# Optimization experiments

Hardware: AMD Instinct MI355X
Metric: run time of the kernel (lower is better)

Reference implementation:

```python
import jax, jax.numpy as jnp
import numpy as np

NS_C = 128
VDW_N = 6.0
MAX_VDW = 0.0356
MIN_VDW = 0.0178
DEV_VDW_RADIUS = 0.2
DM_MIN = 0.5


def _mlp(h, W1, b1, W2, b2):
    # h: [B, Nl, Nt, 2*ns_c] -> [B, Nl, Nt]
    r = jax.nn.relu(jnp.einsum('blnc,ck->blnk', h, W1) + b1)
    return (jnp.einsum('blnk,k->bln', r, W2[:, 0]) + b2[0])


def setup_inputs() -> dict:
    key = jax.random.key(0)
    ks = jax.random.split(key, 16)
    B, Nl, Nt, C = 8, 64, 512, NS_C
    s1 = 1.0 / np.sqrt(2 * C)
    s2 = 1.0 / np.sqrt(C)
    return {
        'ligand_pos': jax.random.normal(ks[0], (B, Nl, 3), jnp.float32),
        'target_pos': jax.random.normal(ks[1], (B, Nt, 3), jnp.float32),
        'ligand_vdw_radii': jax.random.uniform(ks[2], (B, Nl), jnp.float32),
        'target_vdw_radii': jax.random.uniform(ks[3], (B, Nt), jnp.float32),
        'ligand_non_metal': jnp.ones((B, Nl), jnp.float32),
        'target_non_metal': jnp.ones((B, Nt), jnp.float32),
        'interaction_indice': jax.random.uniform(ks[4], (B, 3, Nl, Nt), jnp.float32),
        'rotor': jax.random.uniform(ks[5], (B,), jnp.float32),
        'h_cat': jax.random.normal(ks[6], (B, Nl, Nt, 2 * C), jnp.float32),
        'WA1': jax.random.normal(ks[7], (2 * C, C), jnp.float32) * s1,
        'bA1': jnp.zeros((C,), jnp.float32),
        'WA2': jax.random.normal(ks[8], (C, 1), jnp.float32) * s2,
        'bA2': jnp.zeros((1,), jnp.float32),
        'WB1': jax.random.normal(ks[9], (2 * C, C), jnp.float32) * s1,
        'bB1': jnp.zeros((C,), jnp.float32),
        'WB2': jax.random.normal(ks[10], (C, 1), jnp.float32) * s2,
        'bB2': jnp.zeros((1,), jnp.float32),
        'hbond_coeff': jnp.array([1.0], jnp.float32),
        'hydrophobic_coeff': jnp.array([0.5], jnp.float32),
        'rotor_coeff': jnp.array([0.5], jnp.float32),
    }


def reference(ligand_pos, target_pos, ligand_vdw_radii, target_vdw_radii,
              ligand_non_metal, target_non_metal, interaction_indice, rotor,
              h_cat, WA1, bA1, WA2, bA2, WB1, bB1, WB2, bB2,
              hbond_coeff, hydrophobic_coeff, rotor_coeff):
    # pairwise distance matrix [B, Nl, Nt]
    diff = ligand_pos[:, :, None, :] - target_pos[:, None, :, :]
    dm = jnp.sqrt(jnp.sum(diff * diff, axis=-1) + 1e-10)
    dm = jnp.where(dm < DM_MIN, jnp.float32(1e10), dm)

    # shared pair quantities (computed once, fused)
    Bp = jnp.tanh(_mlp(h_cat, WB1, bB1, WB2, bB2)) * DEV_VDW_RADIUS
    dm_0 = ligand_vdw_radii[:, :, None] + target_vdw_radii[:, None, :] + Bp

    # vdw term
    dm_0c = jnp.where(dm_0 < 1e-4, jnp.float32(1.0), dm_0)
    r6 = (dm_0c / dm) ** VDW_N
    vdw_e = jnp.minimum(r6 * r6 - 2.0 * r6, 100.0)
    vdw_e = vdw_e * ligand_non_metal[:, :, None] * target_non_metal[:, None, :]
    A_vdw = jax.nn.sigmoid(_mlp(h_cat, WA1, bA1, WA2, bA2))
    A_vdw = A_vdw * (MAX_VDW - MIN_VDW) + MIN_VDW
    vdw = jnp.sum(A_vdw * vdw_e, axis=(1, 2))

    d = dm - dm_0

    def hbond_term(A, coeff):
        r = jnp.clip(d * A / -0.7, 0.0, 1.0)
        return jnp.sum(r, axis=(1, 2)) * -(coeff[0] * coeff[0])

    hbond = hbond_term(interaction_indice[:, 0], hbond_coeff)
    metal = hbond_term(interaction_indice[:, 1], hbond_coeff)

    hphob = jnp.clip((-d + 1.5) * interaction_indice[:, 2], 0.0, 1.0)
    hphob = jnp.sum(hphob, axis=(1, 2)) * -(hydrophobic_coeff[0] * hydrophobic_coeff[0])

    energies = jnp.stack([vdw, hbond, metal, hphob], axis=-1)  # [B, 4]
    energies = energies / (1.0 + rotor_coeff[0] * rotor_coeff[0] * rotor[:, None])
    return energies
```

## Files before the change

kernel.cpp:

```cpp
#include <hip/hip_runtime.h>
#include <hip/hip_bf16.h>


typedef _Float16 half8 __attribute__((ext_vector_type(8)));
typedef float    f32x4 __attribute__((ext_vector_type(4)));
typedef unsigned int u32x4 __attribute__((ext_vector_type(4)));

#define NLIG 64
#define NTGT 512
#define KDIM 256
#define NDIM 256
#define BM   128
#define BK   32
#define NKS  8
#define RS   40

__global__ void ed_prep_kernel(const float* __restrict__ WA1,
                               const float* __restrict__ WB1,
                               _Float16* __restrict__ wt,
                               float* __restrict__ out) {
    int gid = blockIdx.x * 256 + threadIdx.x;
    int c   = gid >> 6;
    int n0  = (gid & 63) * 4;
    const float* src = (n0 < 128) ? (WA1 + c * 128 + n0)
                                  : (WB1 + c * 128 + (n0 - 128));
    f32x4 v = *(const f32x4*)src;
#pragma unroll
    for (int j = 0; j < 4; ++j)
        wt[(size_t)(n0 + j) * 256 + c] = (_Float16)v[j];
    if (gid < 32) out[gid] = 0.0f;
}

__global__ __launch_bounds__(512, 4) void ed_main_kernel(
    const float* __restrict__ lig_pos, const float* __restrict__ tgt_pos,
    const float* __restrict__ lig_vdw, const float* __restrict__ tgt_vdw,
    const float* __restrict__ lig_nm,  const float* __restrict__ tgt_nm,
    const float* __restrict__ ind,     const float* __restrict__ rotor,
    const float* __restrict__ h,       const _Float16* __restrict__ wt,
    const float* __restrict__ bA1, const float* __restrict__ WA2,
    const float* __restrict__ bA2,
    const float* __restrict__ bB1, const float* __restrict__ WB2,
    const float* __restrict__ bB2,
    const float* __restrict__ hbc, const float* __restrict__ hpc,
    const float* __restrict__ rtc,
    float* __restrict__ out)
{
    __shared__ _Float16 sA[2][BM * RS];
    __shared__ _Float16 sW[2][NDIM * RS];
    __shared__ float    sRed[4][BM];
    __shared__ float    sFin[32];

    const int tid  = threadIdx.x;
    const int lane = tid & 63;
    const int wid  = tid >> 6;
    const int wm   = wid >> 2;
    const int wn   = wid & 3;
    const int lr   = lane & 15;
    const int lg   = lane >> 4;

    const int bx = blockIdx.x;
    const int b  = bx >> 8;
    const int l  = (bx >> 2) & 63;
    const int t0 = (bx & 3) * BM;

    const float* hA = h + (size_t)bx * (BM * KDIM);

    const int arow = tid >> 2;
    const int akq  = (tid & 3) * 8;
    const int wrow = tid >> 1;
    const int whq  = (tid & 1) * 16;

    f32x4 a0, a1;
    u32x4 w0, w1;

    {
        const float* pa = hA + (size_t)arow * KDIM + akq;
        a0 = *(const f32x4*)pa;
        a1 = *(const f32x4*)(pa + 4);
        const _Float16* pw = wt + wrow * KDIM + whq;
        w0 = *(const u32x4*)pw;
        w1 = *(const u32x4*)(pw + 8);
        half8 hv;
#pragma unroll
        for (int j = 0; j < 4; ++j) hv[j] = (_Float16)a0[j];
#pragma unroll
        for (int j = 0; j < 4; ++j) hv[4 + j] = (_Float16)a1[j];
        *(half8*)&sA[0][arow * RS + akq] = hv;
        *(u32x4*)&sW[0][wrow * RS + whq]     = w0;
        *(u32x4*)&sW[0][wrow * RS + whq + 8] = w1;
    }

    f32x4 acc[4][4];
#pragma unroll
    for (int m = 0; m < 4; ++m)
#pragma unroll
        for (int n = 0; n < 4; ++n) acc[m][n] = 0;

    for (int ks = 0; ks < NKS; ++ks) {
        const int bf = ks & 1;
        __syncthreads();
        if (ks + 1 < NKS) {
            const float* pa = hA + (size_t)arow * KDIM + (ks + 1) * BK + akq;
            a0 = *(const f32x4*)pa;
            a1 = *(const f32x4*)(pa + 4);
            const _Float16* pw = wt + wrow * KDIM + (ks + 1) * BK + whq;
            w0 = *(const u32x4*)pw;
            w1 = *(const u32x4*)(pw + 8);
        }
        half8 af[4], wf[4];
#pragma unroll
        for (int m = 0; m < 4; ++m)
            af[m] = *(const half8*)&sA[bf][(wm * 64 + m * 16 + lr) * RS + lg * 8];
#pragma unroll
        for (int n = 0; n < 4; ++n)
            wf[n] = *(const half8*)&sW[bf][(wn * 64 + n * 16 + lr) * RS + lg * 8];
#pragma unroll
        for (int m = 0; m < 4; ++m)
#pragma unroll
            for (int n = 0; n < 4; ++n)
                acc[m][n] = __builtin_amdgcn_mfma_f32_16x16x32_f16(
                    af[m], wf[n], acc[m][n], 0, 0, 0);
        if (ks + 1 < NKS) {
            const int nb = bf ^ 1;
            half8 hv;
#pragma unroll
            for (int j = 0; j < 4; ++j) hv[j] = (_Float16)a0[j];
#pragma unroll
            for (int j = 0; j < 4; ++j) hv[4 + j] = (_Float16)a1[j];
            *(half8*)&sA[nb][arow * RS + akq] = hv;
            *(u32x4*)&sW[nb][wrow * RS + whq]     = w0;
            *(u32x4*)&sW[nb][wrow * RS + whq + 8] = w1;
        }
    }

    float cb[4], cw[4];
#pragma unroll
    for (int n = 0; n < 4; ++n) {
        int col = wn * 64 + n * 16 + lr;
        if (col < 128) { cb[n] = bA1[col];       cw[n] = WA2[col]; }
        else           { cb[n] = bB1[col - 128]; cw[n] = WB2[col - 128]; }
    }
#pragma unroll
    for (int m = 0; m < 4; ++m) {
#pragma unroll
        for (int r = 0; r < 4; ++r) {
            float p = 0.f;
#pragma unroll
            for (int n = 0; n < 4; ++n)
                p += fmaxf(acc[m][n][r] + cb[n], 0.f) * cw[n];
            p += __shfl_xor(p, 1);
            p += __shfl_xor(p, 2);
            p += __shfl_xor(p, 4);
            p += __shfl_xor(p, 8);
            if (lr == 0)
                sRed[wn][wm * 64 + m * 16 + lg * 4 + r] = p;
        }
    }
    __syncthreads();

    float e0 = 0.f, e1 = 0.f, e2 = 0.f, e3 = 0.f;
    if (tid < BM) {
        const int t = t0 + tid;
        float mlpA = sRed[0][tid] + sRed[1][tid] + bA2[0];
        float mlpB = sRed[2][tid] + sRed[3][tid] + bB2[0];
        float Bp = tanhf(mlpB) * 0.2f;
        float lv = lig_vdw[b * NLIG + l];
        float tv = tgt_vdw[b * NTGT + t];
        float dx = lig_pos[(b * NLIG + l) * 3 + 0] - tgt_pos[(b * NTGT + t) * 3 + 0];
        float dy = lig_pos[(b * NLIG + l) * 3 + 1] - tgt_pos[(b * NTGT + t) * 3 + 1];
        float dz = lig_pos[(b * NLIG + l) * 3 + 2] - tgt_pos[(b * NTGT + t) * 3 + 2];
        float dm = sqrtf(dx * dx + dy * dy + dz * dz + 1e-10f);
        if (dm < 0.5f) dm = 1e10f;
        float dm0  = lv + tv + Bp;
        float dm0c = (dm0 < 1e-4f) ? 1.0f : dm0;
        float qr = dm0c / dm;
        float q2 = qr * qr;
        float r6 = q2 * q2 * q2;
        float ve = fminf(r6 * r6 - 2.0f * r6, 100.0f);
        ve *= lig_nm[b * NLIG + l] * tgt_nm[b * NTGT + t];
        float Av = 1.0f / (1.0f + expf(-mlpA)) * (float)(0.0356 - 0.0178) + 0.0178f;
        e0 = Av * ve;
        float d = dm - dm0;
        const float* ib = ind + (size_t)b * 3 * NLIG * NTGT + (size_t)l * NTGT + t;
        float i0 = ib[0];
        float i1 = ib[NLIG * NTGT];
        float i2 = ib[2 * NLIG * NTGT];
        e1 = fminf(fmaxf(d * i0 / -0.7f, 0.f), 1.f);
        e2 = fminf(fmaxf(d * i1 / -0.7f, 0.f), 1.f);
        e3 = fminf(fmaxf((-d + 1.5f) * i2, 0.f), 1.f);
    }
#pragma unroll
    for (int off = 32; off > 0; off >>= 1) {
        e0 += __shfl_down(e0, off);
        e1 += __shfl_down(e1, off);
        e2 += __shfl_down(e2, off);
        e3 += __shfl_down(e3, off);
    }
    if (lane == 0) {
        sFin[wid * 4 + 0] = e0; sFin[wid * 4 + 1] = e1;
        sFin[wid * 4 + 2] = e2; sFin[wid * 4 + 3] = e3;
    }
    __syncthreads();
    if (tid == 0) {
        float s0 = 0, s1 = 0, s2 = 0, s3 = 0;
#pragma unroll
        for (int w = 0; w < 8; ++w) {
            s0 += sFin[w * 4 + 0]; s1 += sFin[w * 4 + 1];
            s2 += sFin[w * 4 + 2]; s3 += sFin[w * 4 + 3];
        }
        float hc = hbc[0], pc = hpc[0], rc = rtc[0];
        float inv = 1.0f / (1.0f + rc * rc * rotor[b]);
        __hip_atomic_fetch_add(&out[b * 4 + 0], s0 * inv,
                               __ATOMIC_RELAXED, __HIP_MEMORY_SCOPE_AGENT);
        __hip_atomic_fetch_add(&out[b * 4 + 1], -(hc * hc) * s1 * inv,
                               __ATOMIC_RELAXED, __HIP_MEMORY_SCOPE_AGENT);
        __hip_atomic_fetch_add(&out[b * 4 + 2], -(hc * hc) * s2 * inv,
                               __ATOMIC_RELAXED, __HIP_MEMORY_SCOPE_AGENT);
        __hip_atomic_fetch_add(&out[b * 4 + 3], -(pc * pc) * s3 * inv,
                               __ATOMIC_RELAXED, __HIP_MEMORY_SCOPE_AGENT);
    }
}

extern "C" void kernel_launch(void* const* d_in, const int* in_sizes, int n_in,
                              void* d_out, int out_size, void* d_ws, size_t ws_size,
                              hipStream_t stream) {
    (void)in_sizes; (void)n_in; (void)out_size; (void)ws_size;
    const float* lig_pos = (const float*)d_in[0];
    const float* tgt_pos = (const float*)d_in[1];
    const float* lig_vdw = (const float*)d_in[2];
    const float* tgt_vdw = (const float*)d_in[3];
    const float* lig_nm  = (const float*)d_in[4];
    const float* tgt_nm  = (const float*)d_in[5];
    const float* ind     = (const float*)d_in[6];
    const float* rotor   = (const float*)d_in[7];
    const float* h       = (const float*)d_in[8];
    const float* WA1     = (const float*)d_in[9];
    const float* bA1     = (const float*)d_in[10];
    const float* WA2     = (const float*)d_in[11];
    const float* bA2     = (const float*)d_in[12];
    const float* WB1     = (const float*)d_in[13];
    const float* bB1     = (const float*)d_in[14];
    const float* WB2     = (const float*)d_in[15];
    const float* bB2     = (const float*)d_in[16];
    const float* hbc     = (const float*)d_in[17];
    const float* hpc     = (const float*)d_in[18];
    const float* rtc     = (const float*)d_in[19];
    float* out  = (float*)d_out;
    _Float16* wt = (_Float16*)d_ws;

    ed_prep_kernel<<<dim3(64), dim3(256), 0, stream>>>(WA1, WB1, wt, out);
    ed_main_kernel<<<dim3(2048), dim3(512), 0, stream>>>(
        lig_pos, tgt_pos, lig_vdw, tgt_vdw, lig_nm, tgt_nm, ind, rotor, h, wt,
        bA1, WA2, bA2, bB1, WB2, bB2, hbc, hpc, rtc, out);
}
```

Baseline: 463.6 us.

## Drop LDS staging and stream h directly into MFMA registers with 3-deep prefetch

The GEMM no longer stages the h tile and the weights through double-buffered shared memory. Each wave now loads its A fragments straight from global memory into registers, using a three-stage register prefetch, and reads the fp16 weight fragments directly from global memory or cache. Blocks shrink to 256 threads covering 64 target rows, so there are twice as many blocks, and each wave computes a 32x128 tile that covers one full MLP. The aim is to remove LDS traffic and block-wide barriers in a kernel that is bound by memory bandwidth. The cost is redundant weight reads from global memory and higher register pressure.

```diff
diff --git a/kernel.cpp b/kernel.cpp
--- a/kernel.cpp
+++ b/kernel.cpp
@@ -4,16 +4,10 @@
 
 typedef _Float16 half8 __attribute__((ext_vector_type(8)));
 typedef float    f32x4 __attribute__((ext_vector_type(4)));
-typedef unsigned int u32x4 __attribute__((ext_vector_type(4)));
 
 #define NLIG 64
 #define NTGT 512
-#define KDIM 256
-#define NDIM 256
-#define BM   128
-#define BK   32
-#define NKS  8
-#define RS   40
+#define KD   256
 
 __global__ void ed_prep_kernel(const float* __restrict__ WA1,
                                const float* __restrict__ WB1,
@@ -27,11 +21,11 @@
     f32x4 v = *(const f32x4*)src;
 #pragma unroll
     for (int j = 0; j < 4; ++j)
-        wt[(size_t)(n0 + j) * 256 + c] = (_Float16)v[j];
+        wt[(size_t)(n0 + j) * KD + c] = (_Float16)v[j];
     if (gid < 32) out[gid] = 0.0f;
 }
 
-__global__ __launch_bounds__(512, 4) void ed_main_kernel(
+__global__ __launch_bounds__(256, 3) void ed_main_kernel(
     const float* __restrict__ lig_pos, const float* __restrict__ tgt_pos,
     const float* __restrict__ lig_vdw, const float* __restrict__ tgt_vdw,
     const float* __restrict__ lig_nm,  const float* __restrict__ tgt_nm,
@@ -45,124 +39,98 @@
     const float* __restrict__ rtc,
     float* __restrict__ out)
 {
-    __shared__ _Float16 sA[2][BM * RS];
-    __shared__ _Float16 sW[2][NDIM * RS];
-    __shared__ float    sRed[4][BM];
-    __shared__ float    sFin[32];
+    __shared__ float sRed[2][64];
 
     const int tid  = threadIdx.x;
     const int lane = tid & 63;
     const int wid  = tid >> 6;
-    const int wm   = wid >> 2;
-    const int wn   = wid & 3;
+    const int wm   = wid >> 1;
+    const int wn   = wid & 1;
     const int lr   = lane & 15;
     const int lg   = lane >> 4;
 
-    const int bx = blockIdx.x;
-    const int b  = bx >> 8;
-    const int l  = (bx >> 2) & 63;
-    const int t0 = (bx & 3) * BM;
-
-    const float* hA = h + (size_t)bx * (BM * KDIM);
-
-    const int arow = tid >> 2;
-    const int akq  = (tid & 3) * 8;
-    const int wrow = tid >> 1;
-    const int whq  = (tid & 1) * 16;
-
-    f32x4 a0, a1;
-    u32x4 w0, w1;
-
-    {
-        const float* pa = hA + (size_t)arow * KDIM + akq;
-        a0 = *(const f32x4*)pa;
-        a1 = *(const f32x4*)(pa + 4);
-        const _Float16* pw = wt + wrow * KDIM + whq;
-        w0 = *(const u32x4*)pw;
-        w1 = *(const u32x4*)(pw + 8);
-        half8 hv;
-#pragma unroll
-        for (int j = 0; j < 4; ++j) hv[j] = (_Float16)a0[j];
-#pragma unroll
-        for (int j = 0; j < 4; ++j) hv[4 + j] = (_Float16)a1[j];
-        *(half8*)&sA[0][arow * RS + akq] = hv;
-        *(u32x4*)&sW[0][wrow * RS + whq]     = w0;
-        *(u32x4*)&sW[0][wrow * RS + whq + 8] = w1;
-    }
-
-    f32x4 acc[4][4];
-#pragma unroll
-    for (int m = 0; m < 4; ++m)
-#pragma unroll
-        for (int n = 0; n < 4; ++n) acc[m][n] = 0;
-
-    for (int ks = 0; ks < NKS; ++ks) {
-        const int bf = ks & 1;
-        __syncthreads();
-        if (ks + 1 < NKS) {
-            const float* pa = hA + (size_t)arow * KDIM + (ks + 1) * BK + akq;
-            a0 = *(const f32x4*)pa;
-            a1 = *(const f32x4*)(pa + 4);
-            const _Float16* pw = wt + wrow * KDIM + (ks + 1) * BK + whq;
-            w0 = *(const u32x4*)pw;
-            w1 = *(const u32x4*)(pw + 8);
-        }
-        half8 af[4], wf[4];
-#pragma unroll
-        for (int m = 0; m < 4; ++m)
-            af[m] = *(const half8*)&sA[bf][(wm * 64 + m * 16 + lr) * RS + lg * 8];
-#pragma unroll
-        for (int n = 0; n < 4; ++n)
-            wf[n] = *(const half8*)&sW[bf][(wn * 64 + n * 16 + lr) * RS + lg * 8];
-#pragma unroll
-        for (int m = 0; m < 4; ++m)
-#pragma unroll
-            for (int n = 0; n < 4; ++n)
-                acc[m][n] = __builtin_amdgcn_mfma_f32_16x16x32_f16(
-                    af[m], wf[n], acc[m][n], 0, 0, 0);
-        if (ks + 1 < NKS) {
-            const int nb = bf ^ 1;
-            half8 hv;
-#pragma unroll
-            for (int j = 0; j < 4; ++j) hv[j] = (_Float16)a0[j];
-#pragma unroll
-            for (int j = 0; j < 4; ++j) hv[4 + j] = (_Float16)a1[j];
-            *(half8*)&sA[nb][arow * RS + akq] = hv;
-            *(u32x4*)&sW[nb][wrow * RS + whq]     = w0;
-            *(u32x4*)&sW[nb][wrow * RS + whq + 8] = w1;
-        }
-    }
-
-    float cb[4], cw[4];
-#pragma unroll
-    for (int n = 0; n < 4; ++n) {
-        int col = wn * 64 + n * 16 + lr;
-        if (col < 128) { cb[n] = bA1[col];       cw[n] = WA2[col]; }
-        else           { cb[n] = bB1[col - 128]; cw[n] = WB2[col - 128]; }
-    }
-#pragma unroll
-    for (int m = 0; m < 4; ++m) {
+    const int bx  = blockIdx.x;
+    const int b   = bx >> 9;
+    const int rem = bx & 511;
+    const int l   = rem >> 3;
+    const int t0  = (rem & 7) * 64;
+
+    const float* aB0 = h + ((size_t)bx * 64 + wm * 32 + lr) * KD + lg * 8;
+    const float* aB1 = aB0 + 16 * KD;
+    const _Float16* wB = wt + ((size_t)(wn * 128 + lr)) * KD + lg * 8;
+
+    f32x4 acc[2][8];
+#pragma unroll
+    for (int m = 0; m < 2; ++m)
+#pragma unroll
+        for (int n = 0; n < 8; ++n) acc[m][n] = 0;
+
+    f32x4 al[3][2][2];
+
+#pragma unroll
+    for (int p = 0; p < 2; ++p) {
+        al[p][0][0] = *(const f32x4*)(aB0 + p * 32);
+        al[p][0][1] = *(const f32x4*)(aB0 + p * 32 + 4);
+        al[p][1][0] = *(const f32x4*)(aB1 + p * 32);
+        al[p][1][1] = *(const f32x4*)(aB1 + p * 32 + 4);
+    }
+
+#pragma unroll
+    for (int ks = 0; ks < 8; ++ks) {
+        const int cur = ks % 3;
+        const int pre = (ks + 2) % 3;
+        if (ks + 2 < 8) {
+            al[pre][0][0] = *(const f32x4*)(aB0 + (ks + 2) * 32);
+            al[pre][0][1] = *(const f32x4*)(aB0 + (ks + 2) * 32 + 4);
+            al[pre][1][0] = *(const f32x4*)(aB1 + (ks + 2) * 32);
+            al[pre][1][1] = *(const f32x4*)(aB1 + (ks + 2) * 32 + 4);
+        }
+        half8 ah[2];
+#pragma unroll
+        for (int m = 0; m < 2; ++m)
+#pragma unroll
+            for (int j = 0; j < 4; ++j) {
+                ah[m][j]     = (_Float16)al[cur][m][0][j];
+                ah[m][4 + j] = (_Float16)al[cur][m][1][j];
+            }
+#pragma unroll
+        for (int n = 0; n < 8; ++n) {
+            half8 wh = *(const half8*)(wB + (size_t)n * 16 * KD + ks * 32);
+            acc[0][n] = __builtin_amdgcn_mfma_f32_16x16x32_f16(
+                ah[0], wh, acc[0][n], 0, 0, 0);
+            acc[1][n] = __builtin_amdgcn_mfma_f32_16x16x32_f16(
+                ah[1], wh, acc[1][n], 0, 0, 0);
+        }
+    }
+
+    float cb[8], cw[8];
+#pragma unroll
+    for (int n = 0; n < 8; ++n) {
+        int c = n * 16 + lr;
+        cb[n] = wn ? bB1[c] : bA1[c];
+        cw[n] = wn ? WB2[c] : WA2[c];
+    }
+#pragma unroll
+    for (int m = 0; m < 2; ++m)
 #pragma unroll
         for (int r = 0; r < 4; ++r) {
             float p = 0.f;
 #pragma unroll
-            for (int n = 0; n < 4; ++n)
+            for (int n = 0; n < 8; ++n)
                 p += fmaxf(acc[m][n][r] + cb[n], 0.f) * cw[n];
             p += __shfl_xor(p, 1);
             p += __shfl_xor(p, 2);
             p += __shfl_xor(p, 4);
             p += __shfl_xor(p, 8);
             if (lr == 0)
-                sRed[wn][wm * 64 + m * 16 + lg * 4 + r] = p;
-        }
-    }
+                sRed[wn][wm * 32 + m * 16 + lg * 4 + r] = p;
+        }
     __syncthreads();
 
-    float e0 = 0.f, e1 = 0.f, e2 = 0.f, e3 = 0.f;
-    if (tid < BM) {
+    if (tid < 64) {
         const int t = t0 + tid;
-        float mlpA = sRed[0][tid] + sRed[1][tid] + bA2[0];
-        float mlpB = sRed[2][tid] + sRed[3][tid] + bB2[0];
+        float mlpA = sRed[0][tid] + bA2[0];
+        float mlpB = sRed[1][tid] + bB2[0];
         float Bp = tanhf(mlpB) * 0.2f;
         float lv = lig_vdw[b * NLIG + l];
         float tv = tgt_vdw[b * NTGT + t];
@@ -179,45 +147,34 @@
         float ve = fminf(r6 * r6 - 2.0f * r6, 100.0f);
         ve *= lig_nm[b * NLIG + l] * tgt_nm[b * NTGT + t];
         float Av = 1.0f / (1.0f + expf(-mlpA)) * (float)(0.0356 - 0.0178) + 0.0178f;
-        e0 = Av * ve;
+        float e0 = Av * ve;
         float d = dm - dm0;
         const float* ib = ind + (size_t)b * 3 * NLIG * NTGT + (size_t)l * NTGT + t;
         float i0 = ib[0];
         float i1 = ib[NLIG * NTGT];
         float i2 = ib[2 * NLIG * NTGT];
-        e1 = fminf(fmaxf(d * i0 / -0.7f, 0.f), 1.f);
-        e2 = fminf(fmaxf(d * i1 / -0.7f, 0.f), 1.f);
-        e3 = fminf(fmaxf((-d + 1.5f) * i2, 0.f), 1.f);
-    }
-#pragma unroll
-    for (int off = 32; off > 0; off >>= 1) {
-        e0 += __shfl_down(e0, off);
-        e1 += __shfl_down(e1, off);
-        e2 += __shfl_down(e2, off);
-        e3 += __shfl_down(e3, off);
-    }
-    if (lane == 0) {
-        sFin[wid * 4 + 0] = e0; sFin[wid * 4 + 1] = e1;
-        sFin[wid * 4 + 2] = e2; sFin[wid * 4 + 3] = e3;
-    }
-    __syncthreads();
-    if (tid == 0) {
-        float s0 = 0, s1 = 0, s2 = 0, s3 = 0;
-#pragma unroll
-        for (int w = 0; w < 8; ++w) {
-            s0 += sFin[w * 4 + 0]; s1 += sFin[w * 4 + 1];
-            s2 += sFin[w * 4 + 2]; s3 += sFin[w * 4 + 3];
-        }
-        float hc = hbc[0], pc = hpc[0], rc = rtc[0];
-        float inv = 1.0f / (1.0f + rc * rc * rotor[b]);
-        __hip_atomic_fetch_add(&out[b * 4 + 0], s0 * inv,
-                               __ATOMIC_RELAXED, __HIP_MEMORY_SCOPE_AGENT);
-        __hip_atomic_fetch_add(&out[b * 4 + 1], -(hc * hc) * s1 * inv,
-                               __ATOMIC_RELAXED, __HIP_MEMORY_SCOPE_AGENT);
-        __hip_atomic_fetch_add(&out[b * 4 + 2], -(hc * hc) * s2 * inv,
-                               __ATOMIC_RELAXED, __HIP_MEMORY_SCOPE_AGENT);
-        __hip_atomic_fetch_add(&out[b * 4 + 3], -(pc * pc) * s3 * inv,
-                               __ATOMIC_RELAXED, __HIP_MEMORY_SCOPE_AGENT);
+        float e1 = fminf(fmaxf(d * i0 / -0.7f, 0.f), 1.f);
+        float e2 = fminf(fmaxf(d * i1 / -0.7f, 0.f), 1.f);
+        float e3 = fminf(fmaxf((-d + 1.5f) * i2, 0.f), 1.f);
+#pragma unroll
+        for (int off = 32; off > 0; off >>= 1) {
+            e0 += __shfl_down(e0, off);
+            e1 += __shfl_down(e1, off);
+            e2 += __shfl_down(e2, off);
+            e3 += __shfl_down(e3, off);
+        }
+        if (tid == 0) {
+            float hc = hbc[0], pc = hpc[0], rc = rtc[0];
+            float inv = 1.0f / (1.0f + rc * rc * rotor[b]);
+            __hip_atomic_fetch_add(&out[b * 4 + 0], e0 * inv,
+                                   __ATOMIC_RELAXED, __HIP_MEMORY_SCOPE_AGENT);
+            __hip_atomic_fetch_add(&out[b * 4 + 1], -(hc * hc) * e1 * inv,
+                                   __ATOMIC_RELAXED, __HIP_MEMORY_SCOPE_AGENT);
+            __hip_atomic_fetch_add(&out[b * 4 + 2], -(hc * hc) * e2 * inv,
+                                   __ATOMIC_RELAXED, __HIP_MEMORY_SCOPE_AGENT);
+            __hip_atomic_fetch_add(&out[b * 4 + 3], -(pc * pc) * e3 * inv,
+                                   __ATOMIC_RELAXED, __HIP_MEMORY_SCOPE_AGENT);
+        }
     }
 }
 
@@ -245,11 +202,11 @@
     const float* hbc     = (const float*)d_in[17];
     const float* hpc     = (const float*)d_in[18];
     const float* rtc     = (const float*)d_in[19];
-    float* out  = (float*)d_out;
+    float* out   = (float*)d_out;
     _Float16* wt = (_Float16*)d_ws;
 
     ed_prep_kernel<<<dim3(64), dim3(256), 0, stream>>>(WA1, WB1, wt, out);
-    ed_main_kernel<<<dim3(2048), dim3(512), 0, stream>>>(
+    ed_main_kernel<<<dim3(4096), dim3(256), 0, stream>>>(
         lig_pos, tgt_pos, lig_vdw, tgt_vdw, lig_nm, tgt_nm, ind, rotor, h, wt,
         bA1, WA2, bA2, bB1, WB2, bB2, hbc, hpc, rtc, out);
 }
```

Result: slower. 593.6 us (+28.0%).
